# Kernel optimization log

Hardware: AMD Instinct MI355X
Metric: run time of the kernel (lower is better)

## Reference

```python
import jax, jax.numpy as jnp
import numpy as np

NUM_NODES = 2048   # N (spatial)
SEQ_LEN = 512      # T (temporal)
LATENT = 32
LAYERS = 2
SELF_LOOP_EPS = 0.5
B = 4


def setup_inputs() -> dict:
    key = jax.random.key(0)
    k1, k2, k3 = jax.random.split(key, 3)
    NT = NUM_NODES + SEQ_LEN
    X = jax.random.normal(k1, (B, NT, LATENT), dtype=jnp.float32)
    # GraphSAGE-style per-layer weights: self and neighbor transforms + bias
    Ws = jax.random.normal(k2, (LAYERS, LATENT, LATENT), dtype=jnp.float32) * 0.05
    Wn = jax.random.normal(k3, (LAYERS, LATENT, LATENT), dtype=jnp.float32) * 0.05
    b = jnp.zeros((LAYERS, LATENT), dtype=jnp.float32)
    return {"X": X, "Ws": Ws, "Wn": Wn, "b": b}


def build_adj(X):
    # node_embs = concat(spatial, temporal) == X itself
    adj = jnp.einsum('bnf,bmf->bnm', X, X)          # [B, N+T, N+T]
    adj = jnp.tanh(jax.nn.relu(adj))
    NT = X.shape[1]
    adj = adj + SELF_LOOP_EPS * jnp.eye(NT, dtype=adj.dtype)
    return adj


def reference(X, Ws, Wn, b):
    adj = build_adj(X)
    h = X
    # dense weighted aggregation == sparse message passing over nonzero edges,
    # since edge weights are exactly the adjacency values
    for l in range(LAYERS):
        agg = jnp.einsum('bnm,bmd->bnd', adj, h)    # neighbor aggregation
        h = jax.nn.elu(jnp.einsum('bnd,de->bne', h, Ws[l])
                       + jnp.einsum('bnd,de->bne', agg, Wn[l])
                       + b[l])
    return h
```

## Files before the change

### kernel.cpp

```cpp
#include <hip/hip_runtime.h>
#include <math.h>

#define NT 2560
#define DF 32
#define NB 4
#define SELF_EPS 0.5f
#define MS 8
#define MROWS (NT / MS)
#define MT 64
#define MITERS (MROWS / MT)
#define TN 64

typedef __attribute__((ext_vector_type(8))) short bf16x8;
typedef __attribute__((ext_vector_type(4))) float f32x4;

__device__ __forceinline__ unsigned short f2bf(float f) {
    unsigned u = __builtin_bit_cast(unsigned, f);
    u += 0x7fffu + ((u >> 16) & 1u);
    return (unsigned short)(u >> 16);
}

__device__ __forceinline__ float fast_rcp(float x) {
#if __has_builtin(__builtin_amdgcn_rcpf)
    return __builtin_amdgcn_rcpf(x);
#else
    return 1.0f / x;
#endif
}

__device__ __forceinline__ float tanh_relu(float x) {
    x = fmaxf(x, 0.0f);
    float e = __expf(x + x);
    return 1.0f - 2.0f * fast_rcp(e + 1.0f);
}

__global__ __launch_bounds__(256, 4)
void prep(const float* __restrict__ X, float* __restrict__ aggz,
          unsigned short* __restrict__ Xb, unsigned short* __restrict__ XT)
{
    const int bid = blockIdx.x, t = threadIdx.x;
    if (bid < 640) {
        f32x4 z = {0.f, 0.f, 0.f, 0.f};
        ((f32x4*)aggz)[(size_t)bid * 256 + t] = z;
        return;
    }
    __shared__ float sT[32][33];
    const int tile = bid - 640;
    const int b = tile / 80, n0 = (tile % 80) * 32;
    const int row = t >> 3, c4 = (t & 7) * 4;
    const size_t rbase = ((size_t)(b * NT + n0 + row)) * DF + c4;
    const float4 v = *(const float4*)(X + rbase);
    unsigned p0 = (unsigned)f2bf(v.x) | ((unsigned)f2bf(v.y) << 16);
    unsigned p1 = (unsigned)f2bf(v.z) | ((unsigned)f2bf(v.w) << 16);
    *(uint2*)(Xb + rbase) = make_uint2(p0, p1);
    sT[row][c4 + 0] = v.x; sT[row][c4 + 1] = v.y;
    sT[row][c4 + 2] = v.z; sT[row][c4 + 3] = v.w;
    __syncthreads();
    const int d = t >> 3, nq = (t & 7) * 4;
    unsigned q0 = (unsigned)f2bf(sT[nq + 0][d]) | ((unsigned)f2bf(sT[nq + 1][d]) << 16);
    unsigned q1 = (unsigned)f2bf(sT[nq + 2][d]) | ((unsigned)f2bf(sT[nq + 3][d]) << 16);
    *(uint2*)(XT + ((size_t)(b * DF + d)) * NT + n0 + nq) = make_uint2(q0, q1);
}

__global__ __launch_bounds__(256, 4)
void gsage_main(const unsigned short* __restrict__ Xb,
                const unsigned short* __restrict__ HT,
                float* __restrict__ agg)
{
    __shared__ unsigned short XmL[64 * 40];
    __shared__ unsigned short HtL[32 * 72];
    __shared__ unsigned short Ss[4 * 16 * 72];

    const int t = threadIdx.x;
    const int w = t >> 6, lane = t & 63;
    const int q = lane >> 4, c = lane & 15;
    const int n0 = blockIdx.x * TN;
    const int mbase = blockIdx.y * MROWS;
    const int b = blockIdx.z;

    const size_t xbase = (size_t)b * NT * DF;
    const size_t tbase = (size_t)b * DF * NT;

    const bf16x8 bfn = *(const bf16x8*)(Xb + xbase + (size_t)(n0 + w * 16 + c) * DF + q * 8);

    f32x4 acc0 = {0.f, 0.f, 0.f, 0.f};
    f32x4 acc1 = {0.f, 0.f, 0.f, 0.f};

    const int xrow = t >> 2, xseg = t & 3;
    const int hrow = t >> 3, hseg = t & 7;

    uint4 xv = *(const uint4*)(Xb + xbase + (size_t)(mbase + xrow) * DF + xseg * 8);
    uint4 hv = *(const uint4*)(HT + tbase + (size_t)hrow * NT + mbase + hseg * 8);

    const int n_g = n0 + w * 16 + c;
    unsigned short* SsW = Ss + w * (16 * 72);

    for (int it = 0; it < MITERS; ++it) {
        const int m0 = mbase + it * MT;
        __syncthreads();
        *(uint4*)(XmL + xrow * 40 + xseg * 8) = xv;
        *(uint4*)(HtL + hrow * 72 + hseg * 8) = hv;
        if (it + 1 < MITERS) {
            const int m1 = m0 + MT;
            xv = *(const uint4*)(Xb + xbase + (size_t)(m1 + xrow) * DF + xseg * 8);
            hv = *(const uint4*)(HT + tbase + (size_t)hrow * NT + m1 + hseg * 8);
        }
        __syncthreads();

        #pragma unroll
        for (int t4 = 0; t4 < 4; ++t4) {
            const bf16x8 af = *(const bf16x8*)(XmL + (t4 * 16 + c) * 40 + q * 8);
            const f32x4 zero = {0.f, 0.f, 0.f, 0.f};
            f32x4 st = __builtin_amdgcn_mfma_f32_16x16x32_bf16(af, bfn, zero, 0, 0, 0);
            const int m2 = m0 + t4 * 16 + q * 4;
            float v0 = tanh_relu(st[0]); if (n_g == m2 + 0) v0 += SELF_EPS;
            float v1 = tanh_relu(st[1]); if (n_g == m2 + 1) v1 += SELF_EPS;
            float v2 = tanh_relu(st[2]); if (n_g == m2 + 2) v2 += SELF_EPS;
            float v3 = tanh_relu(st[3]); if (n_g == m2 + 3) v3 += SELF_EPS;
            unsigned p0 = (unsigned)f2bf(v0) | ((unsigned)f2bf(v1) << 16);
            unsigned p1 = (unsigned)f2bf(v2) | ((unsigned)f2bf(v3) << 16);
            *(uint2*)(SsW + c * 72 + t4 * 16 + q * 4) = make_uint2(p0, p1);
        }
        asm volatile("s_waitcnt lgkmcnt(0)" ::: "memory");

        #pragma unroll
        for (int kc = 0; kc < 2; ++kc) {
            const bf16x8 sf = *(const bf16x8*)(SsW + c * 72 + kc * 32 + q * 8);
            const bf16x8 h0 = *(const bf16x8*)(HtL + c * 72 + kc * 32 + q * 8);
            const bf16x8 h1 = *(const bf16x8*)(HtL + (16 + c) * 72 + kc * 32 + q * 8);
            acc0 = __builtin_amdgcn_mfma_f32_16x16x32_bf16(sf, h0, acc0, 0, 0, 0);
            acc1 = __builtin_amdgcn_mfma_f32_16x16x32_bf16(sf, h1, acc1, 0, 0, 0);
        }
    }

    float* ap = agg + xbase + (size_t)(n0 + w * 16 + q * 4) * DF + c;
    #pragma unroll
    for (int r = 0; r < 4; ++r) {
        atomicAdd(ap + (size_t)r * DF, acc0[r]);
        atomicAdd(ap + (size_t)r * DF + 16, acc1[r]);
    }
}

__global__ __launch_bounds__(256, 4)
void gsage_epi(const float* __restrict__ Hin, const float* __restrict__ agg,
               const float* __restrict__ Wsl, const float* __restrict__ Wnl,
               const float* __restrict__ bl,
               float* __restrict__ Hout, unsigned short* __restrict__ HTout)
{
    __shared__ float sW[32][33], sN[32][33], sH[32][36], sA[32][36], sT[32][33];
    const int t = threadIdx.x;
    const int n0 = blockIdx.x * 32;
    const int b = blockIdx.y;
    const int row = t >> 3, c4 = (t & 7) * 4;
    const size_t rb = ((size_t)(b * NT + n0 + row)) * DF + c4;
    const float4 hv = *(const float4*)(Hin + rb);
    const float4 av = *(const float4*)(agg + rb);
    const float4 w0 = *(const float4*)(Wsl + row * DF + c4);
    const float4 w1 = *(const float4*)(Wnl + row * DF + c4);
    sH[row][c4+0]=hv.x; sH[row][c4+1]=hv.y; sH[row][c4+2]=hv.z; sH[row][c4+3]=hv.w;
    sA[row][c4+0]=av.x; sA[row][c4+1]=av.y; sA[row][c4+2]=av.z; sA[row][c4+3]=av.w;
    sW[row][c4+0]=w0.x; sW[row][c4+1]=w0.y; sW[row][c4+2]=w0.z; sW[row][c4+3]=w0.w;
    sN[row][c4+0]=w1.x; sN[row][c4+1]=w1.y; sN[row][c4+2]=w1.z; sN[row][c4+3]=w1.w;
    __syncthreads();

    float4 z = make_float4(bl[c4+0], bl[c4+1], bl[c4+2], bl[c4+3]);
    #pragma unroll
    for (int k = 0; k < DF; ++k) {
        const float hk = sH[row][k], ak = sA[row][k];
        z.x += hk * sW[k][c4+0] + ak * sN[k][c4+0];
        z.y += hk * sW[k][c4+1] + ak * sN[k][c4+1];
        z.z += hk * sW[k][c4+2] + ak * sN[k][c4+2];
        z.w += hk * sW[k][c4+3] + ak * sN[k][c4+3];
    }
    z.x = z.x > 0.f ? z.x : __expf(z.x) - 1.f;
    z.y = z.y > 0.f ? z.y : __expf(z.y) - 1.f;
    z.z = z.z > 0.f ? z.z : __expf(z.z) - 1.f;
    z.w = z.w > 0.f ? z.w : __expf(z.w) - 1.f;
    *(float4*)(Hout + rb) = z;

    if (HTout != nullptr) {
        sT[row][c4+0]=z.x; sT[row][c4+1]=z.y; sT[row][c4+2]=z.z; sT[row][c4+3]=z.w;
        __syncthreads();
        const int d = t >> 3, nq = (t & 7) * 4;
        unsigned q0 = (unsigned)f2bf(sT[nq+0][d]) | ((unsigned)f2bf(sT[nq+1][d]) << 16);
        unsigned q1 = (unsigned)f2bf(sT[nq+2][d]) | ((unsigned)f2bf(sT[nq+3][d]) << 16);
        *(uint2*)(HTout + ((size_t)(b * DF + d)) * NT + n0 + nq) = make_uint2(q0, q1);
    }
}

extern "C" void kernel_launch(void* const* d_in, const int* in_sizes, int n_in,
                              void* d_out, int out_size, void* d_ws, size_t ws_size,
                              hipStream_t stream) {
    const float* X  = (const float*)d_in[0];
    const float* Ws = (const float*)d_in[1];
    const float* Wn = (const float*)d_in[2];
    const float* bv = (const float*)d_in[3];
    float* out = (float*)d_out;

    char* ws = (char*)d_ws;
    float* agg1 = (float*)ws;
    float* agg2 = agg1 + (size_t)NB * NT * DF;
    float* h1   = agg2 + (size_t)NB * NT * DF;
    unsigned short* Xb  = (unsigned short*)(ws + 3932160);
    unsigned short* XT  = Xb + (size_t)NB * NT * DF;
    unsigned short* H1T = XT + (size_t)NB * NT * DF;

    prep<<<960, 256, 0, stream>>>(X, agg1, Xb, XT);

    dim3 g(NT / TN, MS, NB);
    gsage_main<<<g, 256, 0, stream>>>(Xb, XT, agg1);
    gsage_epi<<<dim3(NT / 32, NB), 256, 0, stream>>>(X, agg1, Ws, Wn, bv, h1, H1T);
    gsage_main<<<g, 256, 0, stream>>>(Xb, H1T, agg2);
    gsage_epi<<<dim3(NT / 32, NB), 256, 0, stream>>>(h1, agg2, Ws + DF * DF, Wn + DF * DF,
                                                     bv + DF, out, nullptr);
}
```

Measured before the change: 102.6 us.

## Replace atomic aggregation with per-slice partial buffers reduced in epilogue

The main kernel now writes each M-slice's partial aggregation to its own buffer with plain stores instead of float atomicAdds into a shared accumulator. The epilogue sums the eight partials, and the zero-fill blocks in prep are dropped. The tanh uses a raw exp2 builtin with a prescaled argument, and the self-loop diagonal check becomes a tile-level test. The trade is removing atomic contention and the zeroing pass for eight times more partial-buffer traffic in the epilogue.

New measurement: 106.1 us. 1.03x slower.

```diff
diff --git a/kernel.cpp b/kernel.cpp
--- a/kernel.cpp
+++ b/kernel.cpp
@@ -28,24 +28,27 @@
 #endif
 }
 
+__device__ __forceinline__ float fast_exp2(float x) {
+#if __has_builtin(__builtin_amdgcn_exp2f)
+    return __builtin_amdgcn_exp2f(x);
+#else
+    return exp2f(x);
+#endif
+}
+
 __device__ __forceinline__ float tanh_relu(float x) {
-    x = fmaxf(x, 0.0f);
-    float e = __expf(x + x);
+    float m = fmaxf(x, 0.0f);
+    float e = fast_exp2(m * 2.885390082f);
     return 1.0f - 2.0f * fast_rcp(e + 1.0f);
 }
 
 __global__ __launch_bounds__(256, 4)
-void prep(const float* __restrict__ X, float* __restrict__ aggz,
+void prep(const float* __restrict__ X,
           unsigned short* __restrict__ Xb, unsigned short* __restrict__ XT)
 {
-    const int bid = blockIdx.x, t = threadIdx.x;
-    if (bid < 640) {
-        f32x4 z = {0.f, 0.f, 0.f, 0.f};
-        ((f32x4*)aggz)[(size_t)bid * 256 + t] = z;
-        return;
-    }
+    const int t = threadIdx.x;
     __shared__ float sT[32][33];
-    const int tile = bid - 640;
+    const int tile = blockIdx.x;
     const int b = tile / 80, n0 = (tile % 80) * 32;
     const int row = t >> 3, c4 = (t & 7) * 4;
     const size_t rbase = ((size_t)(b * NT + n0 + row)) * DF + c4;
@@ -65,7 +68,7 @@
 __global__ __launch_bounds__(256, 4)
 void gsage_main(const unsigned short* __restrict__ Xb,
                 const unsigned short* __restrict__ HT,
-                float* __restrict__ agg)
+                float* __restrict__ part)
 {
     __shared__ unsigned short XmL[64 * 40];
     __shared__ unsigned short HtL[32 * 72];
@@ -75,7 +78,8 @@
     const int w = t >> 6, lane = t & 63;
     const int q = lane >> 4, c = lane & 15;
     const int n0 = blockIdx.x * TN;
-    const int mbase = blockIdx.y * MROWS;
+    const int slice = blockIdx.y;
+    const int mbase = slice * MROWS;
     const int b = blockIdx.z;
 
     const size_t xbase = (size_t)b * NT * DF;
@@ -112,11 +116,17 @@
             const bf16x8 af = *(const bf16x8*)(XmL + (t4 * 16 + c) * 40 + q * 8);
             const f32x4 zero = {0.f, 0.f, 0.f, 0.f};
             f32x4 st = __builtin_amdgcn_mfma_f32_16x16x32_bf16(af, bfn, zero, 0, 0, 0);
-            const int m2 = m0 + t4 * 16 + q * 4;
-            float v0 = tanh_relu(st[0]); if (n_g == m2 + 0) v0 += SELF_EPS;
-            float v1 = tanh_relu(st[1]); if (n_g == m2 + 1) v1 += SELF_EPS;
-            float v2 = tanh_relu(st[2]); if (n_g == m2 + 2) v2 += SELF_EPS;
-            float v3 = tanh_relu(st[3]); if (n_g == m2 + 3) v3 += SELF_EPS;
+            float v0 = tanh_relu(st[0]);
+            float v1 = tanh_relu(st[1]);
+            float v2 = tanh_relu(st[2]);
+            float v3 = tanh_relu(st[3]);
+            if ((n0 + w * 16 == m0 + t4 * 16) && (q == (c >> 2))) {
+                const int r = c & 3;
+                v0 += (r == 0) ? SELF_EPS : 0.f;
+                v1 += (r == 1) ? SELF_EPS : 0.f;
+                v2 += (r == 2) ? SELF_EPS : 0.f;
+                v3 += (r == 3) ? SELF_EPS : 0.f;
+            }
             unsigned p0 = (unsigned)f2bf(v0) | ((unsigned)f2bf(v1) << 16);
             unsigned p1 = (unsigned)f2bf(v2) | ((unsigned)f2bf(v3) << 16);
             *(uint2*)(SsW + c * 72 + t4 * 16 + q * 4) = make_uint2(p0, p1);
@@ -133,16 +143,17 @@
         }
     }
 
-    float* ap = agg + xbase + (size_t)(n0 + w * 16 + q * 4) * DF + c;
+    float* pp = part + ((size_t)slice * NB) * NT * DF + xbase
+                     + (size_t)(n0 + w * 16 + q * 4) * DF + c;
     #pragma unroll
     for (int r = 0; r < 4; ++r) {
-        atomicAdd(ap + (size_t)r * DF, acc0[r]);
-        atomicAdd(ap + (size_t)r * DF + 16, acc1[r]);
+        pp[(size_t)r * DF]      = acc0[r];
+        pp[(size_t)r * DF + 16] = acc1[r];
     }
 }
 
 __global__ __launch_bounds__(256, 4)
-void gsage_epi(const float* __restrict__ Hin, const float* __restrict__ agg,
+void gsage_epi(const float* __restrict__ Hin, const float* __restrict__ part,
                const float* __restrict__ Wsl, const float* __restrict__ Wnl,
                const float* __restrict__ bl,
                float* __restrict__ Hout, unsigned short* __restrict__ HTout)
@@ -154,7 +165,12 @@
     const int row = t >> 3, c4 = (t & 7) * 4;
     const size_t rb = ((size_t)(b * NT + n0 + row)) * DF + c4;
     const float4 hv = *(const float4*)(Hin + rb);
-    const float4 av = *(const float4*)(agg + rb);
+    float4 av = make_float4(0.f, 0.f, 0.f, 0.f);
+    #pragma unroll
+    for (int s = 0; s < MS; ++s) {
+        const float4 v = *(const float4*)(part + (size_t)s * NB * NT * DF + rb);
+        av.x += v.x; av.y += v.y; av.z += v.z; av.w += v.w;
+    }
     const float4 w0 = *(const float4*)(Wsl + row * DF + c4);
     const float4 w1 = *(const float4*)(Wnl + row * DF + c4);
     sH[row][c4+0]=hv.x; sH[row][c4+1]=hv.y; sH[row][c4+2]=hv.z; sH[row][c4+3]=hv.w;
@@ -198,19 +214,18 @@
     float* out = (float*)d_out;
 
     char* ws = (char*)d_ws;
-    float* agg1 = (float*)ws;
-    float* agg2 = agg1 + (size_t)NB * NT * DF;
-    float* h1   = agg2 + (size_t)NB * NT * DF;
-    unsigned short* Xb  = (unsigned short*)(ws + 3932160);
+    float* part = (float*)ws;
+    float* h1   = part + (size_t)MS * NB * NT * DF;
+    unsigned short* Xb  = (unsigned short*)(ws + 11796480);
     unsigned short* XT  = Xb + (size_t)NB * NT * DF;
     unsigned short* H1T = XT + (size_t)NB * NT * DF;
 
-    prep<<<960, 256, 0, stream>>>(X, agg1, Xb, XT);
+    prep<<<320, 256, 0, stream>>>(X, Xb, XT);
 
     dim3 g(NT / TN, MS, NB);
-    gsage_main<<<g, 256, 0, stream>>>(Xb, XT, agg1);
-    gsage_epi<<<dim3(NT / 32, NB), 256, 0, stream>>>(X, agg1, Ws, Wn, bv, h1, H1T);
-    gsage_main<<<g, 256, 0, stream>>>(Xb, H1T, agg2);
-    gsage_epi<<<dim3(NT / 32, NB), 256, 0, stream>>>(h1, agg2, Ws + DF * DF, Wn + DF * DF,
+    gsage_main<<<g, 256, 0, stream>>>(Xb, XT, part);
+    gsage_epi<<<dim3(NT / 32, NB), 256, 0, stream>>>(X, part, Ws, Wn, bv, h1, H1T);
+    gsage_main<<<g, 256, 0, stream>>>(Xb, H1T, part);
+    gsage_epi<<<dim3(NT / 32, NB), 256, 0, stream>>>(h1, part, Ws + DF * DF, Wn + DF * DF,
                                                      bv + DF, out, nullptr);
 }
```
